# Performance work log

Measured on AMD Instinct MI355X. Metric: run time of the kernel, lower is better.

The kernel has to match this reference:

```python
import jax, jax.numpy as jnp
import numpy as np

B, C, H, W = 16, 384, 64, 64
HEADS = 8


def setup_inputs() -> dict:
    key = jax.random.key(0)
    ks = jax.random.split(key, 8)
    s = 1.0 / np.sqrt(C)
    return {
        "x": jax.random.normal(ks[0], (B, C, H, W), jnp.float32),
        "w1": jax.random.normal(ks[1], (C, C), jnp.float32) * s,
        "b1": jax.random.normal(ks[2], (C,), jnp.float32) * 0.01,
        "w2": jax.random.normal(ks[3], (C, C), jnp.float32) * s,
        "b2": jax.random.normal(ks[4], (C,), jnp.float32) * 0.01,
        "w3": jax.random.normal(ks[5], (C, C), jnp.float32) * s,
        "b3": jax.random.normal(ks[6], (C,), jnp.float32) * 0.01,
        "temperature": jnp.ones((HEADS, 1, 1), jnp.float32),
    }


def _l2norm(v, eps=1e-12):
    # matches F.normalize(dim=-1): v / max(||v||, eps)
    n = jnp.sqrt(jnp.sum(v * v, axis=-1, keepdims=True))
    return v / jnp.maximum(n, eps)


def reference(x, w1, b1, w2, b2, w3, b3, temperature):
    b, c, h, w = x.shape
    n = h * w
    ch = c // HEADS
    xf = x.reshape(b, c, n)  # [b, c, hw]
    # 1x1 convs == channel matmuls
    q = jnp.einsum('oc,bcn->bon', w1, xf) + b1[:, None]
    k = jnp.einsum('oc,bcn->bon', w2, xf) + b2[:, None]
    v = jnp.einsum('oc,bcn->bon', w3, xf) + b3[:, None]
    q = q.reshape(b, HEADS, ch, n)
    k = k.reshape(b, HEADS, ch, n)
    v = v.reshape(b, HEADS, ch, n)
    qn = _l2norm(q)
    kn = _l2norm(k)
    # transposed (channel) attention: [b, head, ch, ch]
    attn = jnp.einsum('bhcn,bhdn->bhcd', qn, kn) * temperature
    attn = jax.nn.softmax(attn, axis=-1)
    # dropout is identity in eval mode
    out = jnp.einsum('bhcd,bhdn->bhcn', attn, v) + v
    out = out.reshape(b, c, h, w) + x
    return out
```

## Files before the change

kernel.cpp:

```cpp
#include <hip/hip_runtime.h>

#define CB 384
#define NB 4096

typedef float f32x4 __attribute__((ext_vector_type(4)));
typedef __bf16 bf16x8 __attribute__((ext_vector_type(8)));

__device__ __forceinline__ void cvt8(const float* __restrict__ src, __bf16* dst) {
  float4 f0 = *(const float4*)src;
  float4 f1 = *(const float4*)(src + 4);
  bf16x8 v = { (__bf16)f0.x, (__bf16)f0.y, (__bf16)f0.z, (__bf16)f0.w,
               (__bf16)f1.x, (__bf16)f1.y, (__bf16)f1.z, (__bf16)f1.w };
  *(bf16x8*)dst = v;
}

__global__ __launch_bounds__(256) void k_xsum(const float* __restrict__ x, float* __restrict__ xsum) {
  const float4* r4 = (const float4*)(x + (size_t)blockIdx.x * NB);
  float s = 0.f;
  for (int j = threadIdx.x; j < NB / 4; j += 256) { float4 f = r4[j]; s += (f.x + f.y) + (f.z + f.w); }
  #pragma unroll
  for (int off = 32; off > 0; off >>= 1) s += __shfl_down(s, off);
  __shared__ float wsum[4];
  if ((threadIdx.x & 63) == 0) wsum[threadIdx.x >> 6] = s;
  __syncthreads();
  if (threadIdx.x == 0) xsum[blockIdx.x] = (wsum[0] + wsum[1]) + (wsum[2] + wsum[3]);
}

__global__ __launch_bounds__(256) void k_wcat(const float* __restrict__ w1, const float* __restrict__ w2,
                                              __bf16* __restrict__ Wc) {
  int i = blockIdx.x * 256 + threadIdx.x;
  float4 f = (i < 36864) ? ((const float4*)w1)[i] : ((const float4*)w2)[i - 36864];
  __bf16* d = Wc + (size_t)i * 4;
  d[0] = (__bf16)f.x; d[1] = (__bf16)f.y; d[2] = (__bf16)f.z; d[3] = (__bf16)f.w;
}

__global__ __launch_bounds__(256) void k_gram_part(const float* __restrict__ x, float* __restrict__ Gpart,
                                                   int chunk) {
  const int TRm[6] = {0, 0, 0, 1, 1, 2};
  const int TCm[6] = {0, 1, 2, 1, 2, 2};
  int t = blockIdx.x, s = blockIdx.y, b = blockIdx.z;
  int tr = TRm[t], tc = TCm[t];
  bool diag = (tr == tc);
  const float* xb = x + (size_t)b * CB * NB;
  __shared__ __align__(16) __bf16 As[128][72];
  __shared__ __align__(16) __bf16 Bs[128][72];
  int tid = threadIdx.x, lane = tid & 63;
  int wr = (tid >> 6) >> 1, wc = (tid >> 6) & 1;
  int rrow = lane & 15, kgrp = lane >> 4;
  f32x4 zero = {0.f, 0.f, 0.f, 0.f};
  f32x4 acc[4][4];
  #pragma unroll
  for (int i = 0; i < 4; ++i)
    #pragma unroll
    for (int j = 0; j < 4; ++j) acc[i][j] = zero;
  int sr = tid >> 1, sh = (tid & 1) * 32;
  const float* pa = xb + (size_t)(tr * 128 + sr) * NB + sh;
  const float* pb = xb + (size_t)(tc * 128 + sr) * NB + sh;
  int kbeg = s * chunk, kend = kbeg + chunk;
  for (int k0 = kbeg; k0 < kend; k0 += 64) {
    #pragma unroll
    for (int j = 0; j < 4; ++j) cvt8(pa + k0 + j * 8, &As[sr][sh + j * 8]);
    if (!diag) {
      #pragma unroll
      for (int j = 0; j < 4; ++j) cvt8(pb + k0 + j * 8, &Bs[sr][sh + j * 8]);
    }
    __syncthreads();
    const __bf16 (*Bsrc)[72] = diag ? As : Bs;
    #pragma unroll
    for (int kk = 0; kk < 2; ++kk) {
      int ko = kk * 32 + kgrp * 8;
      bf16x8 af[4], bg[4];
      #pragma unroll
      for (int i = 0; i < 4; ++i) af[i] = *(const bf16x8*)&As[wr * 64 + i * 16 + rrow][ko];
      #pragma unroll
      for (int j = 0; j < 4; ++j) bg[j] = *(const bf16x8*)&Bsrc[wc * 64 + j * 16 + rrow][ko];
      #pragma unroll
      for (int i = 0; i < 4; ++i)
        #pragma unroll
        for (int j = 0; j < 4; ++j)
          acc[i][j] = __builtin_amdgcn_mfma_f32_16x16x32_bf16(af[i], bg[j], acc[i][j], 0, 0, 0);
    }
    __syncthreads();
  }
  float* gp = Gpart + (((size_t)s * 16 + b) * 6 + t) * 16384;
  #pragma unroll
  for (int i = 0; i < 4; ++i)
    #pragma unroll
    for (int rr = 0; rr < 4; ++rr) {
      int row = wr * 64 + i * 16 + kgrp * 4 + rr;
      #pragma unroll
      for (int j = 0; j < 4; ++j) {
        int col = wc * 64 + j * 16 + rrow;
        gp[(size_t)row * 128 + col] = acc[i][j][rr];
      }
    }
}

__global__ __launch_bounds__(256) void k_gsum(const float* __restrict__ Gpart, __bf16* __restrict__ Gb,
                                              int nsplit) {
  const int TRm[6] = {0, 0, 0, 1, 1, 2};
  const int TCm[6] = {0, 1, 2, 1, 2, 2};
  int b = blockIdx.y;
  int idx = blockIdx.x * 256 + threadIdx.x;
  int t = idx / 16384, ij = idx & 16383;
  int i = ij >> 7, j = ij & 127;
  float s = 0.f;
  #pragma unroll 8
  for (int si = 0; si < nsplit; ++si)
    s += Gpart[(((size_t)si * 16 + b) * 6 + t) * 16384 + ij];
  int r = TRm[t] * 128 + i, c = TCm[t] * 128 + j;
  __bf16 v = (__bf16)s;
  Gb[((size_t)b * CB + r) * CB + c] = v;
  if (TRm[t] != TCm[t]) Gb[((size_t)b * CB + c) * CB + r] = v;
}

__global__ __launch_bounds__(256) void k_wg(const __bf16* __restrict__ Wc, const __bf16* __restrict__ Gb,
                                            float* __restrict__ T) {
  int b = blockIdx.y;
  int tr = blockIdx.x / 3, tc = blockIdx.x % 3;
  __shared__ __align__(16) __bf16 As[128][72];
  __shared__ __align__(16) __bf16 Bs[128][72];
  int tid = threadIdx.x, lane = tid & 63;
  int wr = (tid >> 6) >> 1, wc = (tid >> 6) & 1;
  int rrow = lane & 15, kgrp = lane >> 4;
  f32x4 zero = {0.f, 0.f, 0.f, 0.f};
  f32x4 acc[4][4];
  #pragma unroll
  for (int i = 0; i < 4; ++i)
    #pragma unroll
    for (int j = 0; j < 4; ++j) acc[i][j] = zero;
  int sr = tid >> 1, sh = (tid & 1) * 32;
  const __bf16* pa = Wc + (size_t)(tr * 128 + sr) * CB + sh;
  const __bf16* pb = Gb + (size_t)b * CB * CB + (size_t)(tc * 128 + sr) * CB + sh;
  for (int k0 = 0; k0 < CB; k0 += 64) {
    #pragma unroll
    for (int j = 0; j < 4; ++j) {
      *(bf16x8*)&As[sr][sh + j * 8] = *(const bf16x8*)(pa + k0 + j * 8);
      *(bf16x8*)&Bs[sr][sh + j * 8] = *(const bf16x8*)(pb + k0 + j * 8);
    }
    __syncthreads();
    #pragma unroll
    for (int kk = 0; kk < 2; ++kk) {
      int ko = kk * 32 + kgrp * 8;
      bf16x8 af[4], bg[4];
      #pragma unroll
      for (int i = 0; i < 4; ++i) af[i] = *(const bf16x8*)&As[wr * 64 + i * 16 + rrow][ko];
      #pragma unroll
      for (int j = 0; j < 4; ++j) bg[j] = *(const bf16x8*)&Bs[wc * 64 + j * 16 + rrow][ko];
      #pragma unroll
      for (int i = 0; i < 4; ++i)
        #pragma unroll
        for (int j = 0; j < 4; ++j)
          acc[i][j] = __builtin_amdgcn_mfma_f32_16x16x32_bf16(af[i], bg[j], acc[i][j], 0, 0, 0);
    }
    __syncthreads();
  }
  float* tb = T + (size_t)b * 768 * CB;
  #pragma unroll
  for (int i = 0; i < 4; ++i)
    #pragma unroll
    for (int rr = 0; rr < 4; ++rr) {
      int row = tr * 128 + wr * 64 + i * 16 + kgrp * 4 + rr;
      #pragma unroll
      for (int j = 0; j < 4; ++j) {
        int col = tc * 128 + wc * 64 + j * 16 + rrow;
        tb[(size_t)row * CB + col] = acc[i][j][rr];
      }
    }
}

__global__ __launch_bounds__(256) void k_attn(
    const float* __restrict__ w1, const float* __restrict__ b1,
    const float* __restrict__ w2, const float* __restrict__ b2,
    const float* __restrict__ b3,
    const float* __restrict__ temp, const float* __restrict__ xsum,
    const float* __restrict__ w2full, const float* __restrict__ T,
    float* __restrict__ Aw, float* __restrict__ evec) {
  int b = blockIdx.y, h = blockIdx.x, tid = threadIdx.x;
  int c0 = h * 48;
  __shared__ float xsuml[384];
  __shared__ float cA[48][133];
  __shared__ float cB[48][133];
  __shared__ float Sl[48][49];
  __shared__ float nq[48], nk[48], wx1[48], wx2[48];

  for (int i = tid; i < 384; i += 256) xsuml[i] = xsum[b * CB + i];
  __syncthreads();

  for (int base = 0; base < 96; base += 16) {
    int rr = base + (tid >> 4);
    int lg = tid & 15;
    int r = rr % 48;
    bool isq = rr < 48;
    const float* wrow = (isq ? w1 : w2) + (size_t)(c0 + r) * CB;
    const float* trow = T + ((size_t)b * 768 + (isq ? 0 : 384) + c0 + r) * CB;
    float s1 = 0.f, s2 = 0.f;
    for (int e = lg; e < CB; e += 16) { float w = wrow[e]; s1 += w * xsuml[e]; s2 += w * trow[e]; }
    #pragma unroll
    for (int off = 8; off > 0; off >>= 1) {
      s1 += __shfl_xor(s1, off, 16);
      s2 += __shfl_xor(s2, off, 16);
    }
    if (lg == 0) {
      float bb = (isq ? b1 : b2)[c0 + r];
      float n2 = s2 + 2.f * bb * s1 + 4096.f * bb * bb;
      float nv = fmaxf(sqrtf(fmaxf(n2, 0.f)), 1e-12f);
      if (isq) { wx1[r] = s1; nq[r] = nv; } else { wx2[r] = s1; nk[r] = nv; }
    }
  }
  __syncthreads();

  float sacc[12];
  #pragma unroll
  for (int i = 0; i < 12; ++i) sacc[i] = 0.f;
  int cc = tid % 48, dq = tid / 48;
  for (int ch = 0; ch < 3; ++ch) {
    for (int idx = tid; idx < 1536; idx += 256) {
      int row = idx >> 5, q4 = (idx & 31) * 4;
      float4 fa = *(const float4*)(T + ((size_t)b * 768 + c0 + row) * CB + ch * 128 + q4);
      float4 fw = *(const float4*)(w2full + (size_t)(c0 + row) * CB + ch * 128 + q4);
      cA[row][q4 + 0] = fa.x; cA[row][q4 + 1] = fa.y; cA[row][q4 + 2] = fa.z; cA[row][q4 + 3] = fa.w;
      cB[row][q4 + 0] = fw.x; cB[row][q4 + 1] = fw.y; cB[row][q4 + 2] = fw.z; cB[row][q4 + 3] = fw.w;
    }
    __syncthreads();
    if (tid < 192) {
      for (int e = 0; e < 128; ++e) {
        float av = cA[cc][e];
        #pragma unroll
        for (int i = 0; i < 12; ++i) sacc[i] += av * cB[dq * 12 + i][e];
      }
    }
    __syncthreads();
  }
  if (tid < 192) {
    float b1c = b1[c0 + cc];
    float th = temp[h];
    #pragma unroll
    for (int i = 0; i < 12; ++i) {
      int d = dq * 12 + i;
      float b2d = b2[c0 + d];
      float sraw = sacc[i] + b1c * wx2[d] + b2d * wx1[cc] + 4096.f * b1c * b2d;
      Sl[cc][d] = th * sraw / (nq[cc] * nk[d]);
    }
  }
  __syncthreads();

  if (tid < 48) {
    float m = -1e30f;
    #pragma unroll 4
    for (int d = 0; d < 48; ++d) m = fmaxf(m, Sl[tid][d]);
    float ssum = 0.f;
    #pragma unroll 4
    for (int d = 0; d < 48; ++d) { float p = __expf(Sl[tid][d] - m); Sl[tid][d] = p; ssum += p; }
    float inv = 1.f / ssum;
    float ev = 0.f;
    float* arow = Aw + (((size_t)b * 8 + h) * 48 + tid) * 48;
    #pragma unroll 4
    for (int d = 0; d < 48; ++d) {
      float a_ = Sl[tid][d] * inv;
      arow[d] = a_;
      ev += a_ * b3[c0 + d];
    }
    evec[b * CB + c0 + tid] = b3[c0 + tid] + ev;
  }
}

__global__ __launch_bounds__(256) void k_fb(const float* __restrict__ w3, const float* __restrict__ Aw,
                                            __bf16* __restrict__ Fb) {
  int ch = blockIdx.x, h = blockIdx.y, b = blockIdx.z;
  int c0 = h * 48, tid = threadIdx.x;
  __shared__ float a_s[48][49];
  __shared__ float w_s[48][129];
  const float* ab = Aw + ((size_t)b * 8 + h) * 2304;
  for (int idx = tid; idx < 2304; idx += 256) a_s[idx / 48][idx % 48] = ab[idx];
  for (int idx = tid; idx < 1536; idx += 256) {
    int row = idx >> 5, q4 = (idx & 31) * 4;
    float4 fw = *(const float4*)(w3 + (size_t)(c0 + row) * CB + ch * 128 + q4);
    w_s[row][q4 + 0] = fw.x; w_s[row][q4 + 1] = fw.y; w_s[row][q4 + 2] = fw.z; w_s[row][q4 + 3] = fw.w;
  }
  __syncthreads();
  for (int idx = tid; idx < 6144; idx += 256) {
    int c = idx >> 7, a = idx & 127;
    float acc = w_s[c][a];
    #pragma unroll 8
    for (int d = 0; d < 48; ++d) acc += a_s[c][d] * w_s[d][a];
    int ga = ch * 128 + a;
    float val = acc + ((ga == c0 + c) ? 1.f : 0.f);
    Fb[((size_t)b * CB + c0 + c) * CB + ga] = (__bf16)val;
  }
}

__global__ __launch_bounds__(256) void k_out(const __bf16* __restrict__ Fb, const float* __restrict__ x,
                                             const float* __restrict__ evec, float* __restrict__ out) {
  int b = blockIdx.y;
  int tr = blockIdx.x % 3, tn = blockIdx.x / 3;
  __shared__ __align__(16) __bf16 As[128][72];
  __shared__ __align__(16) __bf16 Bs[128][72];
  int tid = threadIdx.x, lane = tid & 63;
  int wr = (tid >> 6) >> 1, wc = (tid >> 6) & 1;
  int rrow = lane & 15, kgrp = lane >> 4;
  f32x4 zero = {0.f, 0.f, 0.f, 0.f};
  f32x4 acc[4][4];
  #pragma unroll
  for (int i = 0; i < 4; ++i)
    #pragma unroll
    for (int j = 0; j < 4; ++j) acc[i][j] = zero;
  int sr = tid >> 1, sh = (tid & 1) * 32;
  const __bf16* pa = Fb + ((size_t)b * CB + tr * 128 + sr) * CB + sh;
  int ba = tid >> 2, bq = tid & 3;
  const float* pxbase = x + ((size_t)b * CB + ba) * NB + tn * 128 + bq * 32;
  for (int k0 = 0; k0 < CB; k0 += 64) {
    #pragma unroll
    for (int j = 0; j < 4; ++j)
      *(bf16x8*)&As[sr][sh + j * 8] = *(const bf16x8*)(pa + k0 + j * 8);
    const float* px = pxbase + (size_t)k0 * NB;
    #pragma unroll
    for (int j = 0; j < 32; j += 4) {
      float4 f = *(const float4*)(px + j);
      int nl = bq * 32 + j;
      Bs[nl + 0][ba] = (__bf16)f.x; Bs[nl + 1][ba] = (__bf16)f.y;
      Bs[nl + 2][ba] = (__bf16)f.z; Bs[nl + 3][ba] = (__bf16)f.w;
    }
    __syncthreads();
    #pragma unroll
    for (int kk = 0; kk < 2; ++kk) {
      int ko = kk * 32 + kgrp * 8;
      bf16x8 af[4], bg[4];
      #pragma unroll
      for (int i = 0; i < 4; ++i) af[i] = *(const bf16x8*)&As[wr * 64 + i * 16 + rrow][ko];
      #pragma unroll
      for (int j = 0; j < 4; ++j) bg[j] = *(const bf16x8*)&Bs[wc * 64 + j * 16 + rrow][ko];
      #pragma unroll
      for (int i = 0; i < 4; ++i)
        #pragma unroll
        for (int j = 0; j < 4; ++j)
          acc[i][j] = __builtin_amdgcn_mfma_f32_16x16x32_bf16(af[i], bg[j], acc[i][j], 0, 0, 0);
    }
    __syncthreads();
  }
  float* ob = out + (size_t)b * CB * NB;
  #pragma unroll
  for (int i = 0; i < 4; ++i)
    #pragma unroll
    for (int rr = 0; rr < 4; ++rr) {
      int row = tr * 128 + wr * 64 + i * 16 + kgrp * 4 + rr;
      float ev = evec[b * CB + row];
      #pragma unroll
      for (int j = 0; j < 4; ++j) {
        int col = tn * 128 + wc * 64 + j * 16 + rrow;
        ob[(size_t)row * NB + col] = acc[i][j][rr] + ev;
      }
    }
}

extern "C" void kernel_launch(void* const* d_in, const int* in_sizes, int n_in,
                              void* d_out, int out_size, void* d_ws, size_t ws_size,
                              hipStream_t stream) {
  const float* x  = (const float*)d_in[0];
  const float* w1 = (const float*)d_in[1];
  const float* b1 = (const float*)d_in[2];
  const float* w2 = (const float*)d_in[3];
  const float* b2 = (const float*)d_in[4];
  const float* w3 = (const float*)d_in[5];
  const float* b3 = (const float*)d_in[6];
  const float* temp = (const float*)d_in[7];
  float* out = (float*)d_out;

  char* ws = (char*)d_ws;
  float*  xsum  = (float*)(ws);
  __bf16* Wc    = (__bf16*)(ws + 24576);
  __bf16* Gb    = (__bf16*)(ws + 614400);
  float*  T     = (float*)(ws + 5332992);
  __bf16* Fb    = (__bf16*)(ws + 24207360);
  float*  evec  = (float*)(ws + 28925952);
  float*  Aw    = (float*)(ws + 28950528);
  float*  Gpart = (float*)(ws + 30130176);

  const size_t base = 30130176;
  int nsplit = 1;
  if (base + 8ull * 6291456 <= ws_size) nsplit = 8;
  else if (base + 4ull * 6291456 <= ws_size) nsplit = 4;
  else if (base + 2ull * 6291456 <= ws_size) nsplit = 2;

  k_xsum<<<dim3(16 * 384), 256, 0, stream>>>(x, xsum);
  k_wcat<<<dim3(288), 256, 0, stream>>>(w1, w2, Wc);
  k_gram_part<<<dim3(6, nsplit, 16), 256, 0, stream>>>(x, Gpart, NB / nsplit);
  k_gsum<<<dim3(384, 16), 256, 0, stream>>>(Gpart, Gb, nsplit);
  k_wg<<<dim3(18, 16), 256, 0, stream>>>(Wc, Gb, T);
  k_attn<<<dim3(8, 16), 256, 0, stream>>>(w1, b1, w2, b2, b3, temp, xsum, w2, T, Aw, evec);
  k_fb<<<dim3(3, 8, 16), 256, 0, stream>>>(w3, Aw, Fb);
  k_out<<<dim3(96, 16), 256, 0, stream>>>(Fb, x, evec, out);
}
```

Baseline: 414.7 us.

## Pre-convert x to bf16 (plain and transposed) once, reuse in gram and output GEMMs

Adds a kernel that converts x to bf16 in two layouts: row-major, and transposed [b, n, c]. The same kernel computes the channel sums with atomics. The gram and output GEMMs then load bf16 directly instead of reading fp32 and converting per tile, which halves their global reads and removes conversion work from the MFMA loops. The cost is an extra pass that writes roughly 100MB of bf16 copies, plus a larger workspace requirement. The original fp32 path remains as a fallback when the workspace is too small.

New measurement: 390.0 us. -6.0%, faster.

```diff
diff --git a/kernel.cpp b/kernel.cpp
--- a/kernel.cpp
+++ b/kernel.cpp
@@ -5,6 +5,7 @@
 
 typedef float f32x4 __attribute__((ext_vector_type(4)));
 typedef __bf16 bf16x8 __attribute__((ext_vector_type(8)));
+typedef __bf16 bf16x4 __attribute__((ext_vector_type(4)));
 
 __device__ __forceinline__ void cvt8(const float* __restrict__ src, __bf16* dst) {
   float4 f0 = *(const float4*)src;
@@ -14,6 +15,44 @@
   *(bf16x8*)dst = v;
 }
 
+#define XT_PITCH 264
+__global__ __launch_bounds__(256) void k_xbf(const float* __restrict__ x, __bf16* __restrict__ xbf,
+                                             __bf16* __restrict__ xbfT, float* __restrict__ xsum) {
+  int ct = blockIdx.x, nt = blockIdx.y, b = blockIdx.z;
+  int c0 = ct * 64, n0 = nt * 256;
+  __shared__ __bf16 tile[64][XT_PITCH];
+  const float* xb = x + ((size_t)b * CB + c0) * NB + n0;
+  __bf16* yb = xbf + ((size_t)b * CB + c0) * NB + n0;
+  int t = threadIdx.x;
+  #pragma unroll
+  for (int j = 0; j < 16; ++j) {
+    int i = t + 256 * j;
+    int r = i >> 6, c4 = (i & 63) * 4;
+    float4 f = *(const float4*)(xb + (size_t)r * NB + c4);
+    bf16x4 v = { (__bf16)f.x, (__bf16)f.y, (__bf16)f.z, (__bf16)f.w };
+    *(bf16x4*)(yb + (size_t)r * NB + c4) = v;
+    *(bf16x4*)&tile[r][c4] = v;
+  }
+  __syncthreads();
+  {
+    int row = t >> 2, q = t & 3;
+    float s = 0.f;
+    #pragma unroll 8
+    for (int m = 0; m < 64; ++m) s += (float)tile[row][q * 64 + m];
+    s += __shfl_xor(s, 1, 4);
+    s += __shfl_xor(s, 2, 4);
+    if (q == 0) atomicAdd(&xsum[b * CB + c0 + row], s);
+  }
+  __bf16* zb = xbfT + ((size_t)b * NB + n0 + t) * CB + c0;
+  #pragma unroll
+  for (int c8 = 0; c8 < 8; ++c8) {
+    bf16x8 v;
+    #pragma unroll
+    for (int m = 0; m < 8; ++m) v[m] = tile[c8 * 8 + m][t];
+    *(bf16x8*)(zb + c8 * 8) = v;
+  }
+}
+
 __global__ __launch_bounds__(256) void k_xsum(const float* __restrict__ x, float* __restrict__ xsum) {
   const float4* r4 = (const float4*)(x + (size_t)blockIdx.x * NB);
   float s = 0.f;
@@ -34,8 +73,70 @@
   d[0] = (__bf16)f.x; d[1] = (__bf16)f.y; d[2] = (__bf16)f.z; d[3] = (__bf16)f.w;
 }
 
-__global__ __launch_bounds__(256) void k_gram_part(const float* __restrict__ x, float* __restrict__ Gpart,
-                                                   int chunk) {
+__global__ __launch_bounds__(256) void k_gram_bf(const __bf16* __restrict__ xbf, float* __restrict__ Gpart,
+                                                 int chunk) {
+  const int TRm[6] = {0, 0, 0, 1, 1, 2};
+  const int TCm[6] = {0, 1, 2, 1, 2, 2};
+  int t = blockIdx.x, s = blockIdx.y, b = blockIdx.z;
+  int tr = TRm[t], tc = TCm[t];
+  bool diag = (tr == tc);
+  const __bf16* xb = xbf + (size_t)b * CB * NB;
+  __shared__ __align__(16) __bf16 As[128][72];
+  __shared__ __align__(16) __bf16 Bs[128][72];
+  int tid = threadIdx.x, lane = tid & 63;
+  int wr = (tid >> 6) >> 1, wc = (tid >> 6) & 1;
+  int rrow = lane & 15, kgrp = lane >> 4;
+  f32x4 zero = {0.f, 0.f, 0.f, 0.f};
+  f32x4 acc[4][4];
+  #pragma unroll
+  for (int i = 0; i < 4; ++i)
+    #pragma unroll
+    for (int j = 0; j < 4; ++j) acc[i][j] = zero;
+  int sr = tid >> 1, sh = (tid & 1) * 32;
+  const __bf16* pa = xb + (size_t)(tr * 128 + sr) * NB + sh;
+  const __bf16* pb = xb + (size_t)(tc * 128 + sr) * NB + sh;
+  int kbeg = s * chunk, kend = kbeg + chunk;
+  for (int k0 = kbeg; k0 < kend; k0 += 64) {
+    #pragma unroll
+    for (int j = 0; j < 4; ++j) *(bf16x8*)&As[sr][sh + j * 8] = *(const bf16x8*)(pa + k0 + j * 8);
+    if (!diag) {
+      #pragma unroll
+      for (int j = 0; j < 4; ++j) *(bf16x8*)&Bs[sr][sh + j * 8] = *(const bf16x8*)(pb + k0 + j * 8);
+    }
+    __syncthreads();
+    const __bf16 (*Bsrc)[72] = diag ? As : Bs;
+    #pragma unroll
+    for (int kk = 0; kk < 2; ++kk) {
+      int ko = kk * 32 + kgrp * 8;
+      bf16x8 af[4], bg[4];
+      #pragma unroll
+      for (int i = 0; i < 4; ++i) af[i] = *(const bf16x8*)&As[wr * 64 + i * 16 + rrow][ko];
+      #pragma unroll
+      for (int j = 0; j < 4; ++j) bg[j] = *(const bf16x8*)&Bsrc[wc * 64 + j * 16 + rrow][ko];
+      #pragma unroll
+      for (int i = 0; i < 4; ++i)
+        #pragma unroll
+        for (int j = 0; j < 4; ++j)
+          acc[i][j] = __builtin_amdgcn_mfma_f32_16x16x32_bf16(af[i], bg[j], acc[i][j], 0, 0, 0);
+    }
+    __syncthreads();
+  }
+  float* gp = Gpart + (((size_t)s * 16 + b) * 6 + t) * 16384;
+  #pragma unroll
+  for (int i = 0; i < 4; ++i)
+    #pragma unroll
+    for (int rr = 0; rr < 4; ++rr) {
+      int row = wr * 64 + i * 16 + kgrp * 4 + rr;
+      #pragma unroll
+      for (int j = 0; j < 4; ++j) {
+        int col = wc * 64 + j * 16 + rrow;
+        gp[(size_t)row * 128 + col] = acc[i][j][rr];
+      }
+    }
+}
+
+__global__ __launch_bounds__(256) void k_gram_f32(const float* __restrict__ x, float* __restrict__ Gpart,
+                                                  int chunk) {
   const int TRm[6] = {0, 0, 0, 1, 1, 2};
   const int TCm[6] = {0, 1, 2, 1, 2, 2};
   int t = blockIdx.x, s = blockIdx.y, b = blockIdx.z;
@@ -290,8 +391,64 @@
   }
 }
 
-__global__ __launch_bounds__(256) void k_out(const __bf16* __restrict__ Fb, const float* __restrict__ x,
-                                             const float* __restrict__ evec, float* __restrict__ out) {
+__global__ __launch_bounds__(256) void k_out_bf(const __bf16* __restrict__ Fb, const __bf16* __restrict__ xbfT,
+                                                const float* __restrict__ evec, float* __restrict__ out) {
+  int b = blockIdx.y;
+  int tr = blockIdx.x % 3, tn = blockIdx.x / 3;
+  __shared__ __align__(16) __bf16 As[128][72];
+  __shared__ __align__(16) __bf16 Bs[128][72];
+  int tid = threadIdx.x, lane = tid & 63;
+  int wr = (tid >> 6) >> 1, wc = (tid >> 6) & 1;
+  int rrow = lane & 15, kgrp = lane >> 4;
+  f32x4 zero = {0.f, 0.f, 0.f, 0.f};
+  f32x4 acc[4][4];
+  #pragma unroll
+  for (int i = 0; i < 4; ++i)
+    #pragma unroll
+    for (int j = 0; j < 4; ++j) acc[i][j] = zero;
+  int sr = tid >> 1, sh = (tid & 1) * 32;
+  const __bf16* pa = Fb + ((size_t)b * CB + tr * 128 + sr) * CB + sh;
+  const __bf16* pb = xbfT + ((size_t)b * NB + tn * 128 + sr) * CB + sh;
+  for (int k0 = 0; k0 < CB; k0 += 64) {
+    #pragma unroll
+    for (int j = 0; j < 4; ++j) {
+      *(bf16x8*)&As[sr][sh + j * 8] = *(const bf16x8*)(pa + k0 + j * 8);
+      *(bf16x8*)&Bs[sr][sh + j * 8] = *(const bf16x8*)(pb + k0 + j * 8);
+    }
+    __syncthreads();
+    #pragma unroll
+    for (int kk = 0; kk < 2; ++kk) {
+      int ko = kk * 32 + kgrp * 8;
+      bf16x8 af[4], bg[4];
+      #pragma unroll
+      for (int i = 0; i < 4; ++i) af[i] = *(const bf16x8*)&As[wr * 64 + i * 16 + rrow][ko];
+      #pragma unroll
+      for (int j = 0; j < 4; ++j) bg[j] = *(const bf16x8*)&Bs[wc * 64 + j * 16 + rrow][ko];
+      #pragma unroll
+      for (int i = 0; i < 4; ++i)
+        #pragma unroll
+        for (int j = 0; j < 4; ++j)
+          acc[i][j] = __builtin_amdgcn_mfma_f32_16x16x32_bf16(af[i], bg[j], acc[i][j], 0, 0, 0);
+    }
+    __syncthreads();
+  }
+  float* ob = out + (size_t)b * CB * NB;
+  #pragma unroll
+  for (int i = 0; i < 4; ++i)
+    #pragma unroll
+    for (int rr = 0; rr < 4; ++rr) {
+      int row = tr * 128 + wr * 64 + i * 16 + kgrp * 4 + rr;
+      float ev = evec[b * CB + row];
+      #pragma unroll
+      for (int j = 0; j < 4; ++j) {
+        int col = tn * 128 + wc * 64 + j * 16 + rrow;
+        ob[(size_t)row * NB + col] = acc[i][j][rr] + ev;
+      }
+    }
+}
+
+__global__ __launch_bounds__(256) void k_out_f32(const __bf16* __restrict__ Fb, const float* __restrict__ x,
+                                                 const float* __restrict__ evec, float* __restrict__ out) {
   int b = blockIdx.y;
   int tr = blockIdx.x % 3, tn = blockIdx.x / 3;
   __shared__ __align__(16) __bf16 As[128][72];
@@ -367,27 +524,52 @@
   float* out = (float*)d_out;
 
   char* ws = (char*)d_ws;
-  float*  xsum  = (float*)(ws);
-  __bf16* Wc    = (__bf16*)(ws + 24576);
-  __bf16* Gb    = (__bf16*)(ws + 614400);
-  float*  T     = (float*)(ws + 5332992);
-  __bf16* Fb    = (__bf16*)(ws + 24207360);
-  float*  evec  = (float*)(ws + 28925952);
-  float*  Aw    = (float*)(ws + 28950528);
-  float*  Gpart = (float*)(ws + 30130176);
-
-  const size_t base = 30130176;
-  int nsplit = 1;
-  if (base + 8ull * 6291456 <= ws_size) nsplit = 8;
-  else if (base + 4ull * 6291456 <= ws_size) nsplit = 4;
-  else if (base + 2ull * 6291456 <= ws_size) nsplit = 2;
-
-  k_xsum<<<dim3(16 * 384), 256, 0, stream>>>(x, xsum);
-  k_wcat<<<dim3(288), 256, 0, stream>>>(w1, w2, Wc);
-  k_gram_part<<<dim3(6, nsplit, 16), 256, 0, stream>>>(x, Gpart, NB / nsplit);
-  k_gsum<<<dim3(384, 16), 256, 0, stream>>>(Gpart, Gb, nsplit);
-  k_wg<<<dim3(18, 16), 256, 0, stream>>>(Wc, Gb, T);
-  k_attn<<<dim3(8, 16), 256, 0, stream>>>(w1, b1, w2, b2, b3, temp, xsum, w2, T, Aw, evec);
-  k_fb<<<dim3(3, 8, 16), 256, 0, stream>>>(w3, Aw, Fb);
-  k_out<<<dim3(96, 16), 256, 0, stream>>>(Fb, x, evec, out);
-}
+  float*  xsum = (float*)(ws);
+  __bf16* Wc   = (__bf16*)(ws + 24576);
+  __bf16* Gb   = (__bf16*)(ws + 614400);
+  float*  T    = (float*)(ws + 5332992);
+  __bf16* Fb   = (__bf16*)(ws + 24207360);
+  float*  evec = (float*)(ws + 28925952);
+  float*  Aw   = (float*)(ws + 28950528);
+
+  const size_t base = 30130176ull;
+  const size_t XBF_BYTES = 50331648ull;
+  const size_t GP1 = 6291456ull;
+
+  __bf16* xbf  = (__bf16*)(ws + base);
+  __bf16* xbfT = (__bf16*)(ws + base + XBF_BYTES);
+  float*  GpF  = (float*)(ws + base + 2 * XBF_BYTES);
+
+  int nsplit_fast = 0;
+  size_t fbase = base + 2 * XBF_BYTES;
+  if (fbase + 8 * GP1 <= ws_size) nsplit_fast = 8;
+  else if (fbase + 4 * GP1 <= ws_size) nsplit_fast = 4;
+  else if (fbase + 2 * GP1 <= ws_size) nsplit_fast = 2;
+  else if (fbase + 1 * GP1 <= ws_size) nsplit_fast = 1;
+
+  if (nsplit_fast > 0) {
+    hipMemsetAsync(xsum, 0, 24576, stream);
+    k_xbf<<<dim3(6, 16, 16), 256, 0, stream>>>(x, xbf, xbfT, xsum);
+    k_wcat<<<dim3(288), 256, 0, stream>>>(w1, w2, Wc);
+    k_gram_bf<<<dim3(6, nsplit_fast, 16), 256, 0, stream>>>(xbf, GpF, NB / nsplit_fast);
+    k_gsum<<<dim3(384, 16), 256, 0, stream>>>(GpF, Gb, nsplit_fast);
+    k_wg<<<dim3(18, 16), 256, 0, stream>>>(Wc, Gb, T);
+    k_attn<<<dim3(8, 16), 256, 0, stream>>>(w1, b1, w2, b2, b3, temp, xsum, w2, T, Aw, evec);
+    k_fb<<<dim3(3, 8, 16), 256, 0, stream>>>(w3, Aw, Fb);
+    k_out_bf<<<dim3(96, 16), 256, 0, stream>>>(Fb, xbfT, evec, out);
+  } else {
+    float* GpS = (float*)(ws + base);
+    int nsplit = 1;
+    if (base + 8 * GP1 <= ws_size) nsplit = 8;
+    else if (base + 4 * GP1 <= ws_size) nsplit = 4;
+    else if (base + 2 * GP1 <= ws_size) nsplit = 2;
+    k_xsum<<<dim3(16 * 384), 256, 0, stream>>>(x, xsum);
+    k_wcat<<<dim3(288), 256, 0, stream>>>(w1, w2, Wc);
+    k_gram_f32<<<dim3(6, nsplit, 16), 256, 0, stream>>>(x, GpS, NB / nsplit);
+    k_gsum<<<dim3(384, 16), 256, 0, stream>>>(GpS, Gb, nsplit);
+    k_wg<<<dim3(18, 16), 256, 0, stream>>>(Wc, Gb, T);
+    k_attn<<<dim3(8, 16), 256, 0, stream>>>(w1, b1, w2, b2, b3, temp, xsum, w2, T, Aw, evec);
+    k_fb<<<dim3(3, 8, 16), 256, 0, stream>>>(w3, Aw, Fb);
+    k_out_f32<<<dim3(96, 16), 256, 0, stream>>>(Fb, x, evec, out);
+  }
+}
```
